# Kernel tuning notes

Hardware: AMD Instinct MI355X
Metric: run time of the kernel (lower is better)

## Reference

```python
import jax, jax.numpy as jnp
import numpy as np

TEMPERATURE = 0.07
BASE_TEMPERATURE = 1.0
CONF_EMA_M = 0.99


def setup_inputs() -> dict:
    key = jax.random.key(0)
    k1, k2, k3 = jax.random.split(key, 3)
    b, n, q, k = 64, 30000, 32, 100
    return {
        "output": jax.random.normal(k1, (b, b, q, k), dtype=jnp.float32),
        "confidence": jax.random.uniform(k2, (n, q, k), dtype=jnp.float32),
        "batch_index": jax.random.randint(k3, (b,), 0, n, dtype=jnp.int64 if jax.config.read('jax_enable_x64') else jnp.int32),
        "x_mask": jnp.ones((b, q, k), dtype=bool),
        "topk": 3,
    }


def reference(output, confidence, batch_index, x_mask, topk):
    b, _, q, k = output.shape
    # output / T, rearrange 'b1 b2 q k -> b1 q (b2 k)', log-softmax over (b2 k)
    x = output / TEMPERATURE
    x = jnp.transpose(x, (0, 2, 1, 3)).reshape(b, q, b * k)
    x = jax.nn.log_softmax(x, axis=-1)
    atten = jnp.transpose(x.reshape(b, q, b, k), (0, 2, 1, 3))  # [b1,b2,q,k]
    logit = jnp.einsum('iiqk->iqk', atten)  # diagonal over (b1,b2) -> [b,q,k]

    # pseudo target from confidence buffer, masked
    pseudo = jnp.where(x_mask, confidence[batch_index], 0.0)
    # top-k mask along region axis (no-grad in original)
    kk = min(int(topk), k)
    _, idx = jax.lax.top_k(pseudo, kk)  # [b,q,kk]
    bi = jnp.arange(b)[:, None, None]
    qi = jnp.arange(q)[None, :, None]
    tmask = jnp.zeros(pseudo.shape, dtype=bool).at[bi, qi, idx].set(True)
    mask = tmask & x_mask
    pseudo = jnp.where(mask, pseudo, 0.0)
    phrase_mask = mask[:, :, 0]

    eps = jnp.finfo(logit.dtype).eps
    loss = -(pseudo * logit).sum(-1)
    loss = loss.sum() / (phrase_mask.sum() + eps)
    loss = loss * BASE_TEMPERATURE

    # confidence score (no-grad branch): masked softmax over regions
    neg_inf = jnp.finfo(logit.dtype).max
    logit_m = jnp.where(x_mask, logit, -neg_inf)  # in-place masked_fill_ in torch
    conf = jax.nn.softmax(logit_m, axis=-1)
    conf = jnp.where(x_mask, conf, 0.0)

    # hard EMA scatter update of confidence buffer
    hard = jax.nn.one_hot(jnp.argmax(conf, axis=-1), k, dtype=confidence.dtype)
    hard = jnp.where(x_mask, hard, 0.0)
    new_confidence = confidence.at[batch_index].set(
        CONF_EMA_M * confidence[batch_index] + (1.0 - CONF_EMA_M) * hard
    )
    return loss, atten, logit_m, pseudo, conf, new_confidence
```

## Files before the change

### kernel.cpp

```cpp
#include <hip/hip_runtime.h>
#include <float.h>
#include <math.h>

#define Bdim 64
#define Qdim 32
#define Kdim 100
#define QK   (Qdim*Kdim)
#define ROWLEN (Bdim*Kdim)
#define ROWV  (ROWLEN/4)
#define MAIN_BLOCKS (Bdim*Qdim)
#define COPY_BLOCKS 16384

typedef float floatx4 __attribute__((ext_vector_type(4)));

__device__ inline float wred_max(float v){ for(int o=32;o;o>>=1) v=fmaxf(v,__shfl_down(v,o)); return v; }
__device__ inline float wred_sum(float v){ for(int o=32;o;o>>=1) v+=__shfl_down(v,o); return v; }

__global__ __launch_bounds__(256) void conloss_fused(
    const float* __restrict__ out_in, const float* __restrict__ conf_in,
    const int* __restrict__ bidx, const int* __restrict__ xmask,
    const int* __restrict__ topk_p,
    float* __restrict__ atten_o, float* __restrict__ logitm_o,
    float* __restrict__ pseudo_o, float* __restrict__ conf_o,
    float* __restrict__ newconf_o, long long nconf,
    float* __restrict__ acc, int* __restrict__ hard_o)
{
    const int tid = threadIdx.x;

    if (blockIdx.x >= MAIN_BLOCKS) {
        const long long nv = (nconf - 3) >> 2;
        const float* __restrict__ s = conf_in + 3;
        float*       __restrict__ d = newconf_o + 3;
        long long v = (long long)(blockIdx.x - MAIN_BLOCKS)*256 + tid;
        const long long str = (long long)(gridDim.x - MAIN_BLOCKS)*256;
        for (; v < nv; v += str) {
            const long long b = v << 2;
            floatx4 t;
            t.x = __builtin_nontemporal_load(s + b);
            t.y = __builtin_nontemporal_load(s + b + 1);
            t.z = __builtin_nontemporal_load(s + b + 2);
            t.w = __builtin_nontemporal_load(s + b + 3);
            __builtin_nontemporal_store(t, (floatx4*)(d + b));
        }
        if (blockIdx.x == MAIN_BLOCKS) {
            if (tid < 3) newconf_o[tid] = conf_in[tid];
            const long long tb = 3 + (nv << 2);
            const int tcnt = (int)(nconf - tb);
            if (tid >= 3 && tid < 3 + tcnt) {
                const long long ix = tb + (tid - 3);
                newconf_o[ix] = conf_in[ix];
            }
        }
        return;
    }

    const int blk = blockIdx.x;
    const int i   = blk >> 5;
    const int qq  = blk & 31;
    const int base_v = i*(Bdim*QK/4) + qq*(Kdim/4);
    const floatx4* __restrict__ out4 = (const floatx4*)out_in;

    floatx4 vv[7];
    float lmax = -INFINITY;
    #pragma unroll
    for (int c = 0; c < 7; ++c) {
        if (c < 6 || tid < 64) {
            int ve = tid + c*256;
            int j = ve/25, k4 = ve - j*25;
            floatx4 v = out4[base_v + j*(QK/4) + k4];
            v *= (1.0f/0.07f);
            vv[c] = v;
            lmax = fmaxf(lmax, fmaxf(fmaxf(v.x, v.y), fmaxf(v.z, v.w)));
        }
    }
    __shared__ float red[4];
    __shared__ float s_max, s_lse;
    const int wid = tid >> 6, lane = tid & 63;
    float wm = wred_max(lmax);
    if (lane == 0) red[wid] = wm;
    __syncthreads();
    if (tid == 0) s_max = fmaxf(fmaxf(red[0],red[1]), fmaxf(red[2],red[3]));
    __syncthreads();
    const float m = s_max;
    float ls = 0.f;
    #pragma unroll
    for (int c = 0; c < 7; ++c) {
        if (c < 6 || tid < 64) {
            floatx4 v = vv[c];
            ls += expf(v.x-m) + expf(v.y-m) + expf(v.z-m) + expf(v.w-m);
        }
    }
    float wsum = wred_sum(ls);
    if (lane == 0) red[wid] = wsum;
    __syncthreads();
    if (tid == 0) s_lse = m + logf(red[0]+red[1]+red[2]+red[3]);
    __syncthreads();
    const float lse = s_lse;

    __shared__ __align__(16) float sm_logit[Kdim];
    const size_t fbase = (size_t)i*(Bdim*QK) + (size_t)qq*Kdim;
    #pragma unroll
    for (int c = 0; c < 7; ++c) {
        if (c < 6 || tid < 64) {
            int ve = tid + c*256;
            int j = ve/25, k4 = ve - j*25;
            floatx4 a = vv[c] - lse;
            float* ap = atten_o + fbase + (size_t)j*QK + 4*k4;
            __builtin_nontemporal_store(a.x, ap);
            __builtin_nontemporal_store(a.y, ap+1);
            __builtin_nontemporal_store(a.z, ap+2);
            __builtin_nontemporal_store(a.w, ap+3);
            if (j == i) *(floatx4*)&sm_logit[4*k4] = a;
        }
    }
    __syncthreads();

    __shared__ float sm_pseudo[Kdim], sm_lm[Kdim];
    __shared__ float s_cm, s_cs;
    __shared__ unsigned long long s_sel[2];
    const size_t ro = (size_t)i*QK + (size_t)qq*Kdim;
    const int row = bidx[i];
    if (tid < Kdim) {
        int kk = tid;
        bool xm = xmask[ro + kk] != 0;
        float pr = xm ? conf_in[(size_t)row*QK + (size_t)qq*Kdim + kk] : 0.0f;
        sm_pseudo[kk] = pr;
        float lm = xm ? sm_logit[kk] : -FLT_MAX;
        sm_lm[kk] = lm;
        logitm_o[ro + kk] = lm;
    }
    __syncthreads();
    if (tid < 64) {
        const bool has2 = (tid + 64) < Kdim;
        float l0 = sm_lm[tid];
        float l1 = has2 ? sm_lm[tid+64] : -FLT_MAX;
        float cmv = wred_max(fmaxf(l0, l1));
        cmv = __shfl(cmv, 0);
        float es = expf(l0 - cmv) + (has2 ? expf(l1 - cmv) : 0.f);
        float csv = wred_sum(es);
        csv = __shfl(csv, 0);
        if (tid == 0) { s_cm = cmv; s_cs = csv; }
        float av = l0; int ai = tid;
        if (has2 && l1 > av) { av = l1; ai = tid + 64; }
        for (int o = 32; o; o >>= 1) {
            float ov = __shfl_down(av, o); int oi = __shfl_down(ai, o);
            if (ov > av || (ov == av && oi < ai)) { av = ov; ai = oi; }
        }
        if (tid == 0) hard_o[i*Qdim + qq] = ai;
        float p0 = sm_pseudo[tid];
        float p1 = has2 ? sm_pseudo[tid+64] : -INFINITY;
        int kt = *topk_p; if (kt > Kdim) kt = Kdim;
        unsigned long long sel0 = 0ull, sel1 = 0ull;
        float lsum = 0.f;
        for (int t = 0; t < kt; ++t) {
            float rv = p0; int ri = tid;
            if (p1 > rv) { rv = p1; ri = tid + 64; }
            for (int o = 32; o; o >>= 1) {
                float ov = __shfl_down(rv, o); int oi = __shfl_down(ri, o);
                if (ov > rv || (ov == rv && oi < ri)) { rv = ov; ri = oi; }
            }
            const int w = __shfl(ri, 0);
            if (w == tid) p0 = -INFINITY;
            if (has2 && w == tid + 64) p1 = -INFINITY;
            if (tid == 0) {
                if (w < 64) sel0 |= 1ull << w; else sel1 |= 1ull << (w - 64);
                lsum += rv * sm_logit[w];
            }
        }
        if (tid == 0) {
            s_sel[0] = sel0; s_sel[1] = sel1;
            atomicAdd(&acc[0], lsum);
            if (((sel0 & 1ull) != 0) && (xmask[ro] != 0)) atomicAdd(&acc[1], 1.0f);
        }
    }
    __syncthreads();
    if (tid < Kdim) {
        int kk = tid;
        bool xm = xmask[ro + kk] != 0;
        float cv = xm ? expf(sm_lm[kk] - s_cm) / s_cs : 0.f;
        conf_o[ro + kk] = cv;
        bool selb = (kk < 64) ? ((s_sel[0] >> kk) & 1ull) : ((s_sel[1] >> (kk-64)) & 1ull);
        pseudo_o[ro + kk] = selb ? sm_pseudo[kk] : 0.f;
    }
}

__global__ __launch_bounds__(256) void conloss_tail(
    const float* __restrict__ conf_in, const int* __restrict__ bidx,
    const int* __restrict__ xmask, const int* __restrict__ hard,
    float* __restrict__ newconf_o, const float* __restrict__ acc,
    float* __restrict__ loss_o)
{
    const int i = blockIdx.x;
    if (i == Bdim) {
        if (threadIdx.x == 0)
            loss_o[0] = -acc[0] / (acc[1] + 1.1920929e-07f);
        return;
    }
    const int row = bidx[i];
    for (int ii = i+1; ii < Bdim; ++ii) if (bidx[ii] == row) return;
    for (int e = threadIdx.x; e < QK; e += blockDim.x) {
        int qq = e / Kdim, kk = e - qq*Kdim;
        bool xm = xmask[(size_t)i*QK + e] != 0;
        float h = (xm && kk == hard[i*Qdim + qq]) ? 1.0f : 0.0f;
        newconf_o[(size_t)row*QK + e] = 0.99f*conf_in[(size_t)row*QK + e] + 0.01f*h;
    }
}

extern "C" void kernel_launch(void* const* d_in, const int* in_sizes, int n_in,
                              void* d_out, int out_size, void* d_ws, size_t ws_size,
                              hipStream_t stream) {
    const float* out_in  = (const float*)d_in[0];
    const float* conf_in = (const float*)d_in[1];
    const int*   bidx    = (const int*)d_in[2];
    const int*   xmask   = (const int*)d_in[3];
    const int*   topk    = (const int*)d_in[4];

    float* o = (float*)d_out;
    float* loss_o   = o;
    float* atten_o  = o + 1;
    float* logitm_o = atten_o + (size_t)Bdim*Bdim*Qdim*Kdim;
    float* pseudo_o = logitm_o + (size_t)Bdim*Qdim*Kdim;
    float* conf_o   = pseudo_o + (size_t)Bdim*Qdim*Kdim;
    float* newconf_o= conf_o   + (size_t)Bdim*Qdim*Kdim;

    float* acc  = (float*)d_ws;
    int*   hard = (int*)((char*)d_ws + 64);

    const long long nconf = (long long)in_sizes[1];

    hipMemsetAsync(d_ws, 0, 64, stream);
    conloss_fused<<<MAIN_BLOCKS + COPY_BLOCKS, 256, 0, stream>>>(
        out_in, conf_in, bidx, xmask, topk,
        atten_o, logitm_o, pseudo_o, conf_o,
        newconf_o, nconf, acc, hard);
    conloss_tail<<<Bdim + 1, 256, 0, stream>>>(conf_in, bidx, xmask, hard,
                                               newconf_o, acc, loss_o);
}
```

Measured before the change: 736.6 us.

## Fuse EMA scatter into main kernel and replace atomics with per-block partials

Moves the hard-EMA confidence update into the main per-row blocks and makes the bulk copy row-wise, skipping rows that will be overwritten. Loss accumulation uses per-block partial sums reduced by a small single-block kernel instead of atomics, which removes the memset and the separate tail kernel. This saves launches and serialization at the cost of a per-row membership check in the copy path.

```diff
diff --git a/kernel.cpp b/kernel.cpp
--- a/kernel.cpp
+++ b/kernel.cpp
@@ -6,8 +6,6 @@
 #define Qdim 32
 #define Kdim 100
 #define QK   (Qdim*Kdim)
-#define ROWLEN (Bdim*Kdim)
-#define ROWV  (ROWLEN/4)
 #define MAIN_BLOCKS (Bdim*Qdim)
 #define COPY_BLOCKS 16384
 
@@ -23,32 +21,32 @@
     float* __restrict__ atten_o, float* __restrict__ logitm_o,
     float* __restrict__ pseudo_o, float* __restrict__ conf_o,
     float* __restrict__ newconf_o, long long nconf,
-    float* __restrict__ acc, int* __restrict__ hard_o)
+    float* __restrict__ part_l, float* __restrict__ part_p)
 {
     const int tid = threadIdx.x;
 
     if (blockIdx.x >= MAIN_BLOCKS) {
-        const long long nv = (nconf - 3) >> 2;
-        const float* __restrict__ s = conf_in + 3;
-        float*       __restrict__ d = newconf_o + 3;
-        long long v = (long long)(blockIdx.x - MAIN_BLOCKS)*256 + tid;
-        const long long str = (long long)(gridDim.x - MAIN_BLOCKS)*256;
-        for (; v < nv; v += str) {
-            const long long b = v << 2;
-            floatx4 t;
-            t.x = __builtin_nontemporal_load(s + b);
-            t.y = __builtin_nontemporal_load(s + b + 1);
-            t.z = __builtin_nontemporal_load(s + b + 2);
-            t.w = __builtin_nontemporal_load(s + b + 3);
-            __builtin_nontemporal_store(t, (floatx4*)(d + b));
-        }
-        if (blockIdx.x == MAIN_BLOCKS) {
-            if (tid < 3) newconf_o[tid] = conf_in[tid];
-            const long long tb = 3 + (nv << 2);
-            const int tcnt = (int)(nconf - tb);
-            if (tid >= 3 && tid < 3 + tcnt) {
-                const long long ix = tb + (tid - 3);
-                newconf_o[ix] = conf_in[ix];
+        __shared__ int s_bidx[Bdim];
+        if (tid < Bdim) s_bidx[tid] = bidx[tid];
+        __syncthreads();
+        const int nrows = (int)(nconf / QK);
+        for (int r = blockIdx.x - MAIN_BLOCKS; r < nrows; r += COPY_BLOCKS) {
+            bool gathered = false;
+            #pragma unroll
+            for (int t = 0; t < Bdim; ++t) gathered |= (s_bidx[t] == r);
+            if (gathered) continue;
+            const float* __restrict__ sr = conf_in  + (size_t)r*QK;
+            float*       __restrict__ dr = newconf_o + (size_t)r*QK;
+            if (tid < 3)  dr[tid]  = sr[tid];
+            if (tid == 3) dr[QK-1] = sr[QK-1];
+            for (int v = tid; v < (QK-4)/4; v += 256) {
+                const float* sp = sr + 3 + 4*v;
+                floatx4 t;
+                t.x = __builtin_nontemporal_load(sp);
+                t.y = __builtin_nontemporal_load(sp + 1);
+                t.z = __builtin_nontemporal_load(sp + 2);
+                t.w = __builtin_nontemporal_load(sp + 3);
+                __builtin_nontemporal_store(t, (floatx4*)(dr + 3 + 4*v));
             }
         }
         return;
@@ -118,12 +116,15 @@
     __shared__ float sm_pseudo[Kdim], sm_lm[Kdim];
     __shared__ float s_cm, s_cs;
     __shared__ unsigned long long s_sel[2];
+    __shared__ int s_hard, s_ema;
     const size_t ro = (size_t)i*QK + (size_t)qq*Kdim;
     const int row = bidx[i];
+    float cv0 = 0.f;
     if (tid < Kdim) {
         int kk = tid;
         bool xm = xmask[ro + kk] != 0;
-        float pr = xm ? conf_in[(size_t)row*QK + (size_t)qq*Kdim + kk] : 0.0f;
+        cv0 = conf_in[(size_t)row*QK + (size_t)qq*Kdim + kk];
+        float pr = xm ? cv0 : 0.0f;
         sm_pseudo[kk] = pr;
         float lm = xm ? sm_logit[kk] : -FLT_MAX;
         sm_lm[kk] = lm;
@@ -146,7 +147,12 @@
             float ov = __shfl_down(av, o); int oi = __shfl_down(ai, o);
             if (ov > av || (ov == av && oi < ai)) { av = ov; ai = oi; }
         }
-        if (tid == 0) hard_o[i*Qdim + qq] = ai;
+        if (tid == 0) {
+            s_hard = ai;
+            int il = 1;
+            for (int ii = i+1; ii < Bdim; ++ii) if (bidx[ii] == row) { il = 0; break; }
+            s_ema = il;
+        }
         float p0 = sm_pseudo[tid];
         float p1 = has2 ? sm_pseudo[tid+64] : -INFINITY;
         int kt = *topk_p; if (kt > Kdim) kt = Kdim;
@@ -169,40 +175,41 @@
         }
         if (tid == 0) {
             s_sel[0] = sel0; s_sel[1] = sel1;
-            atomicAdd(&acc[0], lsum);
-            if (((sel0 & 1ull) != 0) && (xmask[ro] != 0)) atomicAdd(&acc[1], 1.0f);
+            part_l[blk] = lsum;
+            part_p[blk] = (((sel0 & 1ull) != 0) && (xmask[ro] != 0)) ? 1.0f : 0.0f;
         }
     }
     __syncthreads();
     if (tid < Kdim) {
         int kk = tid;
         bool xm = xmask[ro + kk] != 0;
-        float cv = xm ? expf(sm_lm[kk] - s_cm) / s_cs : 0.f;
-        conf_o[ro + kk] = cv;
+        float cvs = xm ? expf(sm_lm[kk] - s_cm) / s_cs : 0.f;
+        conf_o[ro + kk] = cvs;
         bool selb = (kk < 64) ? ((s_sel[0] >> kk) & 1ull) : ((s_sel[1] >> (kk-64)) & 1ull);
         pseudo_o[ro + kk] = selb ? sm_pseudo[kk] : 0.f;
+        if (s_ema) {
+            float h = (xm && kk == s_hard) ? 1.0f : 0.0f;
+            newconf_o[(size_t)row*QK + (size_t)qq*Kdim + kk] = 0.99f*cv0 + 0.01f*h;
+        }
     }
 }
 
-__global__ __launch_bounds__(256) void conloss_tail(
-    const float* __restrict__ conf_in, const int* __restrict__ bidx,
-    const int* __restrict__ xmask, const int* __restrict__ hard,
-    float* __restrict__ newconf_o, const float* __restrict__ acc,
+__global__ __launch_bounds__(256) void conloss_loss(
+    const float* __restrict__ part_l, const float* __restrict__ part_p,
     float* __restrict__ loss_o)
 {
-    const int i = blockIdx.x;
-    if (i == Bdim) {
-        if (threadIdx.x == 0)
-            loss_o[0] = -acc[0] / (acc[1] + 1.1920929e-07f);
-        return;
-    }
-    const int row = bidx[i];
-    for (int ii = i+1; ii < Bdim; ++ii) if (bidx[ii] == row) return;
-    for (int e = threadIdx.x; e < QK; e += blockDim.x) {
-        int qq = e / Kdim, kk = e - qq*Kdim;
-        bool xm = xmask[(size_t)i*QK + e] != 0;
-        float h = (xm && kk == hard[i*Qdim + qq]) ? 1.0f : 0.0f;
-        newconf_o[(size_t)row*QK + e] = 0.99f*conf_in[(size_t)row*QK + e] + 0.01f*h;
+    const int tid = threadIdx.x;
+    float a = 0.f, b = 0.f;
+    for (int t = tid; t < MAIN_BLOCKS; t += 256) { a += part_l[t]; b += part_p[t]; }
+    __shared__ float ra[4], rb[4];
+    const int wid = tid >> 6, lane = tid & 63;
+    float wa = wred_sum(a), wb = wred_sum(b);
+    if (lane == 0) { ra[wid] = wa; rb[wid] = wb; }
+    __syncthreads();
+    if (tid == 0) {
+        float s = ra[0]+ra[1]+ra[2]+ra[3];
+        float c = rb[0]+rb[1]+rb[2]+rb[3];
+        loss_o[0] = -s / (c + 1.1920929e-07f);
     }
 }
 
@@ -223,16 +230,14 @@
     float* conf_o   = pseudo_o + (size_t)Bdim*Qdim*Kdim;
     float* newconf_o= conf_o   + (size_t)Bdim*Qdim*Kdim;
 
-    float* acc  = (float*)d_ws;
-    int*   hard = (int*)((char*)d_ws + 64);
+    float* part_l = (float*)d_ws;
+    float* part_p = part_l + MAIN_BLOCKS;
 
     const long long nconf = (long long)in_sizes[1];
 
-    hipMemsetAsync(d_ws, 0, 64, stream);
     conloss_fused<<<MAIN_BLOCKS + COPY_BLOCKS, 256, 0, stream>>>(
         out_in, conf_in, bidx, xmask, topk,
         atten_o, logitm_o, pseudo_o, conf_o,
-        newconf_o, nconf, acc, hard);
-    conloss_tail<<<Bdim + 1, 256, 0, stream>>>(conf_in, bidx, xmask, hard,
-                                               newconf_o, acc, loss_o);
+        newconf_o, nconf, part_l, part_p);
+    conloss_loss<<<1, 256, 0, stream>>>(part_l, part_p, loss_o);
 }
```

New measurement: 716.9 us (median of 2 runs). 1.03x faster.
